# Kernel tuning notes

Hardware: AMD Instinct MI355X
Metric: run time of the kernel (lower is better)

Reference implementation:

```python
import jax, jax.numpy as jnp
import numpy as np

B, N, M, D, H = 4, 512, 4096, 256, 8
HD = D // H


def setup_inputs() -> dict:
    key = jax.random.key(0)
    ks = jax.random.split(key, 10)
    s = 1.0 / np.sqrt(D)
    return {
        "amr_feats": jax.random.normal(ks[0], (B, N, D), jnp.float32),
        "amr_pad_mask": jax.random.randint(ks[1], (B, N), 0, 2) == 1,
        "visual_feats": jax.random.normal(ks[2], (B, M, D), jnp.float32),
        "W_amr_qk": jax.random.normal(ks[3], (D, D), jnp.float32) * s,
        "W_amr_v": jax.random.normal(ks[4], (D, D), jnp.float32) * s,
        "W_vis_qk": jax.random.normal(ks[5], (D, D), jnp.float32) * s,
        "W_vis_v": jax.random.normal(ks[6], (D, D), jnp.float32) * s,
        "W_amr_out": jax.random.normal(ks[7], (D, D), jnp.float32) * s,
        "b_amr_out": jnp.zeros((D,), jnp.float32),
        "W_vis_out": jax.random.normal(ks[8], (D, D), jnp.float32) * s,
        "b_vis_out": jnp.zeros((D,), jnp.float32),
    }


def _split_heads(x):  # [b, s, d] -> [b, h, s, hd]
    b, s, _ = x.shape
    return x.reshape(b, s, H, HD).transpose(0, 2, 1, 3)


def _merge_heads(x):  # [b, h, s, hd] -> [b, s, d]
    b, _, s, _ = x.shape
    return x.transpose(0, 2, 1, 3).reshape(b, s, H * HD)


def reference(amr_feats, amr_pad_mask, visual_feats,
              W_amr_qk, W_amr_v, W_vis_qk, W_vis_v,
              W_amr_out, b_amr_out, W_vis_out, b_vis_out):
    scale = HD ** -0.5
    amr_qk = _split_heads(amr_feats @ W_amr_qk)      # [b,h,n,hd]
    vis_qk = _split_heads(visual_feats @ W_vis_qk)   # [b,h,m,hd]
    amr_v = _split_heads(amr_feats @ W_amr_v)        # [b,h,n,hd]
    vis_v = _split_heads(visual_feats @ W_vis_v)     # [b,h,m,hd]

    # shared score matrix, computed once and reused for both directions
    common = jnp.einsum('bhnc,bhmc->bhnm', amr_qk, vis_qk) * scale  # [b,h,n,m]

    # amr -> visual (visual_pads is None in the top-level forward: no mask)
    amr_vis_w = jax.nn.softmax(common, axis=-1)
    amr_feats_2 = _merge_heads(jnp.einsum('bhnm,bhmc->bhnc', amr_vis_w, vis_v))
    amr_feats_2 = amr_feats_2 @ W_amr_out + b_amr_out

    # visual -> amr, masked by amr_pad_mask
    neg = jnp.finfo(common.dtype).min
    vis_txt = jnp.where(amr_pad_mask[:, None, None, :], neg,
                        common.transpose(0, 1, 3, 2))  # [b,h,m,n]
    vis_txt_w = jax.nn.softmax(vis_txt, axis=-1)
    visual_feats_2 = _merge_heads(jnp.einsum('bhmn,bhnc->bhmc', vis_txt_w, amr_v))
    visual_feats_2 = visual_feats_2 @ W_vis_out + b_vis_out

    # text_trans == 'dot', visual_trans == 'dot'
    return amr_feats_2 * amr_feats, visual_feats * visual_feats_2
```

## Files before the change

kernel.cpp:

```cpp
#include <hip/hip_runtime.h>

#define BB 4
#define NN 512
#define MM 4096
#define DD 256
#define HH 8
#define HDD 32

typedef __attribute__((ext_vector_type(8))) short bf16x8;
typedef __attribute__((ext_vector_type(4))) float f32x4;
typedef __attribute__((ext_vector_type(4))) unsigned int u32x4;

__device__ __forceinline__ unsigned short f2b(float f) {
    union { float f; unsigned u; } v; v.f = f;
    unsigned r = v.u + 0x7fffu + ((v.u >> 16) & 1u);
    return (unsigned short)(r >> 16);
}
__device__ __forceinline__ float b2f(unsigned short u) {
    union { unsigned u; float f; } v; v.u = ((unsigned)u) << 16;
    return v.f;
}
__device__ __forceinline__ unsigned cvt_pk_bf16(float lo, float hi) {
    unsigned r;
    asm("v_cvt_pk_bf16_f32 %0, %1, %2" : "=v"(r) : "v"(lo), "v"(hi));
    return r;
}

struct WPack { const float* s[6]; unsigned short* d[6]; };
__global__ __launch_bounds__(256) void convert_w(WPack p)
{
    __shared__ unsigned short T[64][72];
    const int mat = blockIdx.x >> 4;
    const int tile = blockIdx.x & 15;
    const int kt = (tile >> 2) * 64, ct = (tile & 3) * 64;
    const int t = threadIdx.x;
    const int kl = t >> 2, cseg = (t & 3) * 16;

    const float* src = &p.s[mat][(size_t)(kt + kl) * DD + ct + cseg];
    #pragma unroll
    for (int j4 = 0; j4 < 4; ++j4) {
        const float4 f = *(const float4*)(src + j4 * 4);
        T[cseg + j4 * 4 + 0][kl] = f2b(f.x);
        T[cseg + j4 * 4 + 1][kl] = f2b(f.y);
        T[cseg + j4 * 4 + 2][kl] = f2b(f.z);
        T[cseg + j4 * 4 + 3][kl] = f2b(f.w);
    }
    __syncthreads();
    unsigned short* dst = &p.d[mat][(size_t)(ct + kl) * DD + kt + cseg];
    *(bf16x8*)dst       = *(const bf16x8*)&T[kl][cseg];
    *(bf16x8*)(dst + 8) = *(const bf16x8*)&T[kl][cseg + 8];
}

template<int OUTMODE>
__device__ __forceinline__ void gemm_tile_in(
    const float* __restrict__ A,
    const unsigned short* __restrict__ Wt,
    float outscale,
    unsigned short* __restrict__ Cb,
    unsigned short* __restrict__ VT, int SEQ,
    int r0, int c0,
    unsigned short (*As)[72], unsigned short (*Ws)[72])
{
    const int tid = threadIdx.x;
    const int lane = tid & 63, w = tid >> 6;
    const int rq = (w >> 1) * 32, cq = (w & 1) * 32;
    const int srow = tid >> 2, skc = (tid & 3) * 16;
    const int g = lane >> 4, cl = lane & 15;

    f32x4 acc[2][2] = {};

    for (int ks = 0; ks < DD; ks += 64) {
        __syncthreads();
        {
            const float* ga = &A[(size_t)(r0 + srow) * DD + ks + skc];
            const float4 f0 = *(const float4*)(ga);
            const float4 f1 = *(const float4*)(ga + 4);
            const float4 f2 = *(const float4*)(ga + 8);
            const float4 f3 = *(const float4*)(ga + 12);
            uint4 u0, u1;
            u0.x = cvt_pk_bf16(f0.x, f0.y); u0.y = cvt_pk_bf16(f0.z, f0.w);
            u0.z = cvt_pk_bf16(f1.x, f1.y); u0.w = cvt_pk_bf16(f1.z, f1.w);
            u1.x = cvt_pk_bf16(f2.x, f2.y); u1.y = cvt_pk_bf16(f2.z, f2.w);
            u1.z = cvt_pk_bf16(f3.x, f3.y); u1.w = cvt_pk_bf16(f3.z, f3.w);
            *(uint4*)&As[srow][skc]     = u0;
            *(uint4*)&As[srow][skc + 8] = u1;
            const unsigned short* gw = &Wt[(size_t)(c0 + srow) * DD + ks + skc];
            *(bf16x8*)&Ws[srow][skc]     = *(const bf16x8*)gw;
            *(bf16x8*)&Ws[srow][skc + 8] = *(const bf16x8*)(gw + 8);
        }
        __syncthreads();
        #pragma unroll
        for (int kh = 0; kh < 2; ++kh) {
            const int kk = kh * 32 + g * 8;
            const bf16x8 a0 = *(const bf16x8*)&As[rq + cl][kk];
            const bf16x8 a1 = *(const bf16x8*)&As[rq + 16 + cl][kk];
            const bf16x8 b0 = *(const bf16x8*)&Ws[cq + cl][kk];
            const bf16x8 b1 = *(const bf16x8*)&Ws[cq + 16 + cl][kk];
            acc[0][0] = __builtin_amdgcn_mfma_f32_16x16x32_bf16(a0, b0, acc[0][0], 0, 0, 0);
            acc[0][1] = __builtin_amdgcn_mfma_f32_16x16x32_bf16(a0, b1, acc[0][1], 0, 0, 0);
            acc[1][0] = __builtin_amdgcn_mfma_f32_16x16x32_bf16(a1, b0, acc[1][0], 0, 0, 0);
            acc[1][1] = __builtin_amdgcn_mfma_f32_16x16x32_bf16(a1, b1, acc[1][1], 0, 0, 0);
        }
    }

    if (OUTMODE == 0) {
        const int b0 = r0 / SEQ, mbase = r0 % SEQ;
        #pragma unroll
        for (int sr = 0; sr < 2; ++sr)
        #pragma unroll
        for (int sc = 0; sc < 2; ++sc) {
            const int col = c0 + cq + sc * 16 + cl;
            const int head = col >> 5, c32 = col & 31;
            #pragma unroll
            for (int reg = 0; reg < 4; ++reg) {
                const int m = mbase + rq + sr * 16 + g * 4 + reg;
                Cb[(((size_t)b0 * HH + head) * SEQ + m) * 32 + c32]
                    = f2b(acc[sr][sc][reg] * outscale);
            }
        }
    } else {
        __syncthreads();
        #pragma unroll
        for (int sr = 0; sr < 2; ++sr)
        #pragma unroll
        for (int sc = 0; sc < 2; ++sc) {
            const int col_local = cq + sc * 16 + cl;
            uint2 u;
            u.x = cvt_pk_bf16(acc[sr][sc][0], acc[sr][sc][1]);
            u.y = cvt_pk_bf16(acc[sr][sc][2], acc[sr][sc][3]);
            *(uint2*)&As[col_local][rq + g * 8 + sr * 4] = u;
        }
        __syncthreads();
        const int col = tid >> 2, seg = tid & 3;
        const int b = r0 / SEQ, m0 = r0 % SEQ;
        unsigned short* dst = &VT[((size_t)b * DD + c0 + col) * SEQ + m0 + seg * 16];
        *(bf16x8*)dst       = *(const bf16x8*)&As[col][seg * 16];
        *(bf16x8*)(dst + 8) = *(const bf16x8*)&As[col][seg * 16 + 8];
    }
}

struct InPack {
    const float* amr; const float* vis;
    const unsigned short *Wqa, *Wva, *Wqv, *Wvv;
    unsigned short *amr_qk, *vis_qk, *VTa, *VTv;
    float sqs;
};
__global__ __launch_bounds__(256) void gemm_in(InPack p)
{
    __shared__ unsigned short As[64][72];
    __shared__ unsigned short Ws[64][72];
    const int bx = blockIdx.x;
    const int c0 = blockIdx.y * 64;
    if (bx < 32)
        gemm_tile_in<0>(p.amr, p.Wqa, p.sqs, p.amr_qk, nullptr, NN, bx * 64, c0, As, Ws);
    else if (bx < 64)
        gemm_tile_in<2>(p.amr, p.Wva, 1.f, nullptr, p.VTa, NN, (bx - 32) * 64, c0, As, Ws);
    else if (bx < 320)
        gemm_tile_in<0>(p.vis, p.Wqv, p.sqs, p.vis_qk, nullptr, MM, (bx - 64) * 64, c0, As, Ws);
    else
        gemm_tile_in<2>(p.vis, p.Wvv, 1.f, nullptr, p.VTv, MM, (bx - 320) * 64, c0, As, Ws);
}

__device__ __forceinline__ void gemm_tile_out(
    const unsigned short* __restrict__ A,
    const unsigned short* __restrict__ Wt,
    const float* __restrict__ bias,
    const float* __restrict__ feats,
    float* __restrict__ Cf,
    int r0, int c0,
    unsigned short (*As)[72], unsigned short (*Ws)[72])
{
    const int tid = threadIdx.x;
    const int lane = tid & 63, w = tid >> 6;
    const int rq = (w >> 1) * 32, cq = (w & 1) * 32;
    const int srow = tid >> 2, skc = (tid & 3) * 16;
    const int g = lane >> 4, cl = lane & 15;

    f32x4 acc[2][2] = {};

    for (int ks = 0; ks < DD; ks += 64) {
        __syncthreads();
        {
            const unsigned short* ga = &A[(size_t)(r0 + srow) * DD + ks + skc];
            *(bf16x8*)&As[srow][skc]     = *(const bf16x8*)ga;
            *(bf16x8*)&As[srow][skc + 8] = *(const bf16x8*)(ga + 8);
            const unsigned short* gw = &Wt[(size_t)(c0 + srow) * DD + ks + skc];
            *(bf16x8*)&Ws[srow][skc]     = *(const bf16x8*)gw;
            *(bf16x8*)&Ws[srow][skc + 8] = *(const bf16x8*)(gw + 8);
        }
        __syncthreads();
        #pragma unroll
        for (int kh = 0; kh < 2; ++kh) {
            const int kk = kh * 32 + g * 8;
            const bf16x8 a0 = *(const bf16x8*)&As[rq + cl][kk];
            const bf16x8 a1 = *(const bf16x8*)&As[rq + 16 + cl][kk];
            const bf16x8 b0 = *(const bf16x8*)&Ws[cq + cl][kk];
            const bf16x8 b1 = *(const bf16x8*)&Ws[cq + 16 + cl][kk];
            acc[0][0] = __builtin_amdgcn_mfma_f32_16x16x32_bf16(a0, b0, acc[0][0], 0, 0, 0);
            acc[0][1] = __builtin_amdgcn_mfma_f32_16x16x32_bf16(a0, b1, acc[0][1], 0, 0, 0);
            acc[1][0] = __builtin_amdgcn_mfma_f32_16x16x32_bf16(a1, b0, acc[1][0], 0, 0, 0);
            acc[1][1] = __builtin_amdgcn_mfma_f32_16x16x32_bf16(a1, b1, acc[1][1], 0, 0, 0);
        }
    }

    #pragma unroll
    for (int sr = 0; sr < 2; ++sr)
    #pragma unroll
    for (int sc = 0; sc < 2; ++sc) {
        const int col = c0 + cq + sc * 16 + cl;
        #pragma unroll
        for (int reg = 0; reg < 4; ++reg) {
            const int row = r0 + rq + sr * 16 + g * 4 + reg;
            const size_t idx = (size_t)row * DD + col;
            Cf[idx] = (acc[sr][sc][reg] + bias[col]) * feats[idx];
        }
    }
}

struct OutPack {
    const unsigned short* A[2];
    const unsigned short* Wt[2];
    const float* bias[2];
    const float* feats[2];
    float* O[2];
};
__global__ __launch_bounds__(256) void gemm_out(OutPack p)
{
    __shared__ unsigned short As[64][72];
    __shared__ unsigned short Ws[64][72];
    const int bx = blockIdx.x;
    const int which = (bx < 32) ? 0 : 1;
    const int rb = (bx < 32) ? bx : bx - 32;
    gemm_tile_out(p.A[which], p.Wt[which], p.bias[which], p.feats[which],
                  p.O[which], rb * 64, blockIdx.y * 64, As, Ws);
}

template<int SEQK, int SPLIT, bool HAS_MASK>
__device__ __forceinline__ void attn_body(
    int bid,
    const unsigned short* __restrict__ Qb,
    const unsigned short* __restrict__ Kb,
    const unsigned short* __restrict__ VTb,
    const int* __restrict__ mask,
    unsigned short* __restrict__ ctx,
    float* __restrict__ Pl, unsigned short* __restrict__ PaccB,
    int NQ, float* maskadd)
{
    constexpr int KCHUNK = SEQK / SPLIT;
    constexpr int NT = KCHUNK / 64;

    const int tid = threadIdx.x;
    const int lane = tid & 63, w = tid >> 6;
    const int g = lane >> 4, cl = lane & 15;

    const int nqt = NQ / 256;
    int bi = bid;
    const int sp = bi % SPLIT; bi /= SPLIT;
    const int qt = bi % nqt;   bi /= nqt;
    const int h  = bi % HH;
    const int b  = bi / HH;
    const int q0 = qt * 256 + w * 64;
    const int kv0 = sp * KCHUNK;

    if (HAS_MASK) {
        for (int i = tid; i < SEQK; i += 256)
            maskadd[i] = mask[b * SEQK + i] ? -1e30f : 0.f;
        __syncthreads();
    }

    bf16x8 aq[4];
    #pragma unroll
    for (int qg = 0; qg < 4; ++qg)
        aq[qg] = *(const bf16x8*)
            &Qb[(((size_t)b * HH + h) * NQ + q0 + qg * 16 + cl) * 32 + g * 8];

    const unsigned short* Kp0 = Kb + (((size_t)b * HH + h) * SEQK + kv0 + cl) * 32 + g * 8;
    const unsigned short* Vp0 = VTb + ((size_t)b * DD + h * HDD + cl) * SEQK + kv0 + g * 8;

    float lsum[4] = {0.f, 0.f, 0.f, 0.f};
    f32x4 acc[4][2] = {};

    bf16x8 Kc[4], Kn[4];
    #pragma unroll
    for (int kf = 0; kf < 4; ++kf)
        Kc[kf] = *(const bf16x8*)(Kp0 + (size_t)(kf * 16) * 32);

    for (int t = 0; t < NT; ++t) {
        const int m0 = kv0 + t * 64;

        if (t + 1 < NT) {
            const unsigned short* kp = Kp0 + (size_t)((t + 1) * 64) * 32;
            #pragma unroll
            for (int kf = 0; kf < 4; ++kf)
                Kn[kf] = *(const bf16x8*)(kp + (size_t)(kf * 16) * 32);
        }

        bf16x8 vv[2][2];
        #pragma unroll
        for (int mh = 0; mh < 2; ++mh)
            #pragma unroll
            for (int sub = 0; sub < 2; ++sub)
                vv[mh][sub] = *(const bf16x8*)
                    (Vp0 + (size_t)(sub * 16) * SEQK + t * 64 + mh * 32);

        uint2 X[4][4];
        #pragma unroll
        for (int kh = 0; kh < 2; ++kh) {
            f32x4 s[4][2];
            #pragma unroll
            for (int k2 = 0; k2 < 2; ++k2) {
                const f32x4 z = {0.f, 0.f, 0.f, 0.f};
                const bf16x8 kfrag = Kc[kh * 2 + k2];
                #pragma unroll
                for (int qg = 0; qg < 4; ++qg)
                    s[qg][k2] = __builtin_amdgcn_mfma_f32_16x16x32_bf16(
                        kfrag, aq[qg], z, 0, 0, 0);
            }
            #pragma unroll
            for (int k2 = 0; k2 < 2; ++k2) {
                const int kf = kh * 2 + k2;
                f32x4 madd;
                if (HAS_MASK)
                    madd = *(const f32x4*)&maskadd[m0 + kf * 16 + g * 4];
                #pragma unroll
                for (int qg = 0; qg < 4; ++qg) {
                    const float p0 = exp2f(s[qg][k2][0] + (HAS_MASK ? madd[0] : 0.f));
                    const float p1 = exp2f(s[qg][k2][1] + (HAS_MASK ? madd[1] : 0.f));
                    const float p2 = exp2f(s[qg][k2][2] + (HAS_MASK ? madd[2] : 0.f));
                    const float p3 = exp2f(s[qg][k2][3] + (HAS_MASK ? madd[3] : 0.f));
                    lsum[qg] += (p0 + p1) + (p2 + p3);
                    X[qg][kf].x = cvt_pk_bf16(p0, p1);
                    X[qg][kf].y = cvt_pk_bf16(p2, p3);
                }
            }
        }

        #pragma unroll
        for (int mh = 0; mh < 2; ++mh) {
            union { u32x4 u; bf16x8 b; } pa[4];
            #pragma unroll
            for (int qg = 0; qg < 4; ++qg) {
                pa[qg].u[0] = X[qg][mh * 2].x;
                pa[qg].u[1] = X[qg][mh * 2].y;
                pa[qg].u[2] = X[qg][mh * 2 + 1].x;
                pa[qg].u[3] = X[qg][mh * 2 + 1].y;
            }
            #pragma unroll
            for (int sub = 0; sub < 2; ++sub)
                #pragma unroll
                for (int qg = 0; qg < 4; ++qg)
                    acc[qg][sub] = __builtin_amdgcn_mfma_f32_16x16x32_bf16(
                        pa[qg].b, vv[mh][sub], acc[qg][sub], 0, 0, 0);
        }

        #pragma unroll
        for (int kf = 0; kf < 4; ++kf) Kc[kf] = Kn[kf];
    }

    #pragma unroll
    for (int qg = 0; qg < 4; ++qg) {
        lsum[qg] += __shfl_xor(lsum[qg], 16);
        lsum[qg] += __shfl_xor(lsum[qg], 32);
    }

    if (SPLIT > 1) {
        const int pb = bid;
        #pragma unroll
        for (int qg = 0; qg < 4; ++qg) {
            #pragma unroll
            for (int sub = 0; sub < 2; ++sub)
                #pragma unroll
                for (int reg = 0; reg < 4; ++reg) {
                    const int wq = w * 64 + qg * 16 + g * 4 + reg;
                    PaccB[((size_t)pb * 256 + wq) * 32 + sub * 16 + cl]
                        = f2b(acc[qg][sub][reg]);
                }
            if (g == 0)
                Pl[(size_t)pb * 256 + w * 64 + qg * 16 + cl] = lsum[qg];
        }
    } else {
        float linv[4][4];
        #pragma unroll
        for (int qg = 0; qg < 4; ++qg)
            #pragma unroll
            for (int reg = 0; reg < 4; ++reg)
                linv[qg][reg] = __shfl(lsum[qg], g * 4 + reg);
        #pragma unroll
        for (int qg = 0; qg < 4; ++qg)
            #pragma unroll
            for (int sub = 0; sub < 2; ++sub)
                #pragma unroll
                for (int reg = 0; reg < 4; ++reg) {
                    const int q = q0 + qg * 16 + g * 4 + reg;
                    ctx[((size_t)b * NQ + q) * DD + h * HDD + sub * 16 + cl]
                        = f2b(acc[qg][sub][reg] / linv[qg][reg]);
                }
    }
}

__global__ __launch_bounds__(256) void attn_fused(
    const unsigned short* __restrict__ amr_qk,
    const unsigned short* __restrict__ vis_qk,
    const unsigned short* __restrict__ VT_vis,
    const unsigned short* __restrict__ VT_amr,
    const int* __restrict__ mask,
    unsigned short* __restrict__ ctx1,
    float* __restrict__ Pl, unsigned short* __restrict__ PaccB)
{
    __shared__ float maskadd[NN];
    if ((blockIdx.x & 1) == 0) {
        attn_body<MM, 8, false>(blockIdx.x >> 1, amr_qk, vis_qk, VT_vis, nullptr,
                                nullptr, Pl, PaccB, NN, maskadd);
    } else {
        attn_body<NN, 1, true>(blockIdx.x >> 1, vis_qk, amr_qk, VT_amr, mask,
                               ctx1, nullptr, nullptr, MM, maskadd);
    }
}

__global__ __launch_bounds__(256) void combine_split(
    const float* __restrict__ Pl, const unsigned short* __restrict__ PaccB,
    unsigned short* __restrict__ ctx)
{
    const int q = threadIdx.x;
    const int bqt = blockIdx.x;
    const int qt = bqt & 1, h = (bqt >> 1) & 7, b = bqt >> 4;
    const int pb0 = bqt * 8;

    float denom = 0.f;
    float o[32] = {};
    #pragma unroll
    for (int sp = 0; sp < 8; ++sp) {
        const size_t base = ((size_t)(pb0 + sp) * 256 + q) * 32;
        #pragma unroll
        for (int c8 = 0; c8 < 4; ++c8) {
            const bf16x8 a = *(const bf16x8*)&PaccB[base + c8 * 8];
            #pragma unroll
            for (int j = 0; j < 8; ++j)
                o[c8 * 8 + j] += b2f((unsigned short)a[j]);
        }
        denom += Pl[(size_t)(pb0 + sp) * 256 + q];
    }
    const float inv = 1.f / denom;

    unsigned short* dst = &ctx[((size_t)b * NN + qt * 256 + q) * DD + h * HDD];
    #pragma unroll
    for (int j4 = 0; j4 < 8; ++j4) {
        ushort4 u;
        u.x = f2b(o[j4 * 4 + 0] * inv); u.y = f2b(o[j4 * 4 + 1] * inv);
        u.z = f2b(o[j4 * 4 + 2] * inv); u.w = f2b(o[j4 * 4 + 3] * inv);
        *(ushort4*)(dst + j4 * 4) = u;
    }
}

extern "C" void kernel_launch(void* const* d_in, const int* in_sizes, int n_in,
                              void* d_out, int out_size, void* d_ws, size_t ws_size,
                              hipStream_t stream)
{
    const float* amr_feats    = (const float*)d_in[0];
    const int*   amr_pad_mask = (const int*)d_in[1];
    const float* visual_feats = (const float*)d_in[2];
    const float* W_amr_qk     = (const float*)d_in[3];
    const float* W_amr_v      = (const float*)d_in[4];
    const float* W_vis_qk     = (const float*)d_in[5];
    const float* W_vis_v      = (const float*)d_in[6];
    const float* W_amr_out    = (const float*)d_in[7];
    const float* b_amr_out    = (const float*)d_in[8];
    const float* W_vis_out    = (const float*)d_in[9];
    const float* b_vis_out    = (const float*)d_in[10];

    unsigned short* ws = (unsigned short*)d_ws;
    unsigned short* Wt_amr_qk  = ws;
    unsigned short* Wt_amr_v   = ws + 65536;
    unsigned short* Wt_vis_qk  = ws + 131072;
    unsigned short* Wt_vis_v   = ws + 196608;
    unsigned short* Wt_amr_out = ws + 262144;
    unsigned short* Wt_vis_out = ws + 327680;
    unsigned short* amr_qk_b   = ws + 393216;
    unsigned short* VT_amr     = ws + 917504;
    unsigned short* vis_qk_b   = ws + 1441792;
    unsigned short* VT_vis     = ws + 5636096;
    unsigned short* ctx0_b     = ws + 9830400;
    unsigned short* ctx1_b     = ws + 10354688;
    float* Pl                  = (float*)(ws + 14548992);
    unsigned short* PaccB      = ws + 15073280;

    float* out0 = (float*)d_out;
    float* out1 = out0 + (size_t)BB * NN * DD;

    const float SQS = 0.50500976f;

    WPack wp;
    wp.s[0] = W_amr_qk;  wp.d[0] = Wt_amr_qk;
    wp.s[1] = W_amr_v;   wp.d[1] = Wt_amr_v;
    wp.s[2] = W_vis_qk;  wp.d[2] = Wt_vis_qk;
    wp.s[3] = W_vis_v;   wp.d[3] = Wt_vis_v;
    wp.s[4] = W_amr_out; wp.d[4] = Wt_amr_out;
    wp.s[5] = W_vis_out; wp.d[5] = Wt_vis_out;
    convert_w<<<96, 256, 0, stream>>>(wp);

    InPack ip;
    ip.amr = amr_feats; ip.vis = visual_feats;
    ip.Wqa = Wt_amr_qk; ip.Wva = Wt_amr_v;
    ip.Wqv = Wt_vis_qk; ip.Wvv = Wt_vis_v;
    ip.amr_qk = amr_qk_b; ip.vis_qk = vis_qk_b;
    ip.VTa = VT_amr; ip.VTv = VT_vis;
    ip.sqs = SQS;
    gemm_in<<<dim3(576, 4), 256, 0, stream>>>(ip);

    attn_fused<<<1024, 256, 0, stream>>>(
        amr_qk_b, vis_qk_b, VT_vis, VT_amr, amr_pad_mask, ctx1_b, Pl, PaccB);
    combine_split<<<64, 256, 0, stream>>>(Pl, PaccB, ctx0_b);

    OutPack op;
    op.A[0] = ctx0_b; op.Wt[0] = Wt_amr_out; op.bias[0] = b_amr_out;
    op.feats[0] = amr_feats;    op.O[0] = out0;
    op.A[1] = ctx1_b; op.Wt[1] = Wt_vis_out; op.bias[1] = b_vis_out;
    op.feats[1] = visual_feats; op.O[1] = out1;
    gemm_out<<<dim3(288, 4), 256, 0, stream>>>(op);
}
```

Before: 94.35 us.

## Compute softmax row sums via MFMA with keep vector and pre-mask V rows

Replaces the scalar per-lane accumulation of exp values and the cross-lane shuffle reduction with an extra MFMA per tile that multiplies P by a bf16 ones (or keep-mask) fragment, so the denominator comes out of the matrix unit. Masking of padded keys moves out of the attention loop: V rows for padded tokens are zeroed in the input GEMM, and a permuted bf16 keep vector built by an extra grid column supplies the masked denominator. This removes the shared-memory mask table, its sync and the per-element mask adds, at the cost of extra MFMAs, a global load per tile, and denominators summed from bf16-rounded probabilities.

```diff
diff --git a/kernel.cpp b/kernel.cpp
--- a/kernel.cpp
+++ b/kernel.cpp
@@ -58,6 +58,7 @@
     float outscale,
     unsigned short* __restrict__ Cb,
     unsigned short* __restrict__ VT, int SEQ,
+    const int* __restrict__ rowmask,
     int r0, int c0,
     unsigned short (*As)[72], unsigned short (*Ws)[72])
 {
@@ -119,6 +120,18 @@
             }
         }
     } else {
+        const int b0 = r0 / SEQ, mbase = r0 % SEQ;
+        if (rowmask != nullptr) {
+            #pragma unroll
+            for (int sr = 0; sr < 2; ++sr)
+                #pragma unroll
+                for (int reg = 0; reg < 4; ++reg) {
+                    const int m = mbase + rq + sr * 16 + g * 4 + reg;
+                    const float k = rowmask[b0 * SEQ + m] ? 0.f : 1.f;
+                    acc[sr][0][reg] *= k;
+                    acc[sr][1][reg] *= k;
+                }
+        }
         __syncthreads();
         #pragma unroll
         for (int sr = 0; sr < 2; ++sr)
@@ -132,8 +145,7 @@
         }
         __syncthreads();
         const int col = tid >> 2, seg = tid & 3;
-        const int b = r0 / SEQ, m0 = r0 % SEQ;
-        unsigned short* dst = &VT[((size_t)b * DD + c0 + col) * SEQ + m0 + seg * 16];
+        unsigned short* dst = &VT[((size_t)b0 * DD + c0 + col) * SEQ + mbase + seg * 16];
         *(bf16x8*)dst       = *(const bf16x8*)&As[col][seg * 16];
         *(bf16x8*)(dst + 8) = *(const bf16x8*)&As[col][seg * 16 + 8];
     }
@@ -143,6 +155,8 @@
     const float* amr; const float* vis;
     const unsigned short *Wqa, *Wva, *Wqv, *Wvv;
     unsigned short *amr_qk, *vis_qk, *VTa, *VTv;
+    const int* mask;
+    unsigned short* keepP;
     float sqs;
 };
 __global__ __launch_bounds__(256) void gemm_in(InPack p)
@@ -152,13 +166,24 @@
     const int bx = blockIdx.x;
     const int c0 = blockIdx.y * 64;
     if (bx < 32)
-        gemm_tile_in<0>(p.amr, p.Wqa, p.sqs, p.amr_qk, nullptr, NN, bx * 64, c0, As, Ws);
+        gemm_tile_in<0>(p.amr, p.Wqa, p.sqs, p.amr_qk, nullptr, NN, nullptr, bx * 64, c0, As, Ws);
     else if (bx < 64)
-        gemm_tile_in<2>(p.amr, p.Wva, 1.f, nullptr, p.VTa, NN, (bx - 32) * 64, c0, As, Ws);
+        gemm_tile_in<2>(p.amr, p.Wva, 1.f, nullptr, p.VTa, NN, p.mask, (bx - 32) * 64, c0, As, Ws);
     else if (bx < 320)
-        gemm_tile_in<0>(p.vis, p.Wqv, p.sqs, p.vis_qk, nullptr, MM, (bx - 64) * 64, c0, As, Ws);
-    else
-        gemm_tile_in<2>(p.vis, p.Wvv, 1.f, nullptr, p.VTv, MM, (bx - 320) * 64, c0, As, Ws);
+        gemm_tile_in<0>(p.vis, p.Wqv, p.sqs, p.vis_qk, nullptr, MM, nullptr, (bx - 64) * 64, c0, As, Ws);
+    else if (bx < 576)
+        gemm_tile_in<2>(p.vis, p.Wvv, 1.f, nullptr, p.VTv, MM, nullptr, (bx - 320) * 64, c0, As, Ws);
+    else if (blockIdx.y == 0) {
+        #pragma unroll
+        for (int k8 = 0; k8 < 8; ++k8) {
+            const int idx = k8 * 256 + threadIdx.x;
+            const int m = idx & (NN - 1);
+            const int r = m & 31;
+            const int pp = ((r & 15) >> 2) * 8 + (r >> 4) * 4 + (r & 3);
+            p.keepP[(idx & ~(NN - 1)) | (m & ~31) | pp]
+                = p.mask[idx] ? (unsigned short)0 : (unsigned short)0x3F80;
+        }
+    }
 }
 
 __device__ __forceinline__ void gemm_tile_out(
@@ -235,16 +260,16 @@
                   p.O[which], rb * 64, blockIdx.y * 64, As, Ws);
 }
 
-template<int SEQK, int SPLIT, bool HAS_MASK>
+template<int SEQK, int SPLIT, bool HAS_KEEP>
 __device__ __forceinline__ void attn_body(
     int bid,
     const unsigned short* __restrict__ Qb,
     const unsigned short* __restrict__ Kb,
     const unsigned short* __restrict__ VTb,
-    const int* __restrict__ mask,
+    const unsigned short* __restrict__ keepP,
     unsigned short* __restrict__ ctx,
     float* __restrict__ Pl, unsigned short* __restrict__ PaccB,
-    int NQ, float* maskadd)
+    int NQ)
 {
     constexpr int KCHUNK = SEQK / SPLIT;
     constexpr int NT = KCHUNK / 64;
@@ -262,12 +287,6 @@
     const int q0 = qt * 256 + w * 64;
     const int kv0 = sp * KCHUNK;
 
-    if (HAS_MASK) {
-        for (int i = tid; i < SEQK; i += 256)
-            maskadd[i] = mask[b * SEQK + i] ? -1e30f : 0.f;
-        __syncthreads();
-    }
-
     bf16x8 aq[4];
     #pragma unroll
     for (int qg = 0; qg < 4; ++qg)
@@ -276,9 +295,14 @@
 
     const unsigned short* Kp0 = Kb + (((size_t)b * HH + h) * SEQK + kv0 + cl) * 32 + g * 8;
     const unsigned short* Vp0 = VTb + ((size_t)b * DD + h * HDD + cl) * SEQK + kv0 + g * 8;
-
-    float lsum[4] = {0.f, 0.f, 0.f, 0.f};
+    const unsigned short* Op0 = HAS_KEEP ? (keepP + (size_t)b * SEQK + kv0 + g * 8) : nullptr;
+
+    union { u32x4 u; bf16x8 b; } onesc;
+    onesc.u[0] = 0x3F803F80u; onesc.u[1] = 0x3F803F80u;
+    onesc.u[2] = 0x3F803F80u; onesc.u[3] = 0x3F803F80u;
+
     f32x4 acc[4][2] = {};
+    f32x4 acc_l[4] = {};
 
     bf16x8 Kc[4], Kn[4];
     #pragma unroll
@@ -286,8 +310,6 @@
         Kc[kf] = *(const bf16x8*)(Kp0 + (size_t)(kf * 16) * 32);
 
     for (int t = 0; t < NT; ++t) {
-        const int m0 = kv0 + t * 64;
-
         if (t + 1 < NT) {
             const unsigned short* kp = Kp0 + (size_t)((t + 1) * 64) * 32;
             #pragma unroll
@@ -302,6 +324,15 @@
             for (int sub = 0; sub < 2; ++sub)
                 vv[mh][sub] = *(const bf16x8*)
                     (Vp0 + (size_t)(sub * 16) * SEQK + t * 64 + mh * 32);
+
+        bf16x8 ofrag[2];
+        if (HAS_KEEP) {
+            ofrag[0] = *(const bf16x8*)(Op0 + t * 64);
+            ofrag[1] = *(const bf16x8*)(Op0 + t * 64 + 32);
+        } else {
+            ofrag[0] = onesc.b;
+            ofrag[1] = onesc.b;
+        }
 
         uint2 X[4][4];
         #pragma unroll
@@ -319,16 +350,12 @@
             #pragma unroll
             for (int k2 = 0; k2 < 2; ++k2) {
                 const int kf = kh * 2 + k2;
-                f32x4 madd;
-                if (HAS_MASK)
-                    madd = *(const f32x4*)&maskadd[m0 + kf * 16 + g * 4];
                 #pragma unroll
                 for (int qg = 0; qg < 4; ++qg) {
-                    const float p0 = exp2f(s[qg][k2][0] + (HAS_MASK ? madd[0] : 0.f));
-                    const float p1 = exp2f(s[qg][k2][1] + (HAS_MASK ? madd[1] : 0.f));
-                    const float p2 = exp2f(s[qg][k2][2] + (HAS_MASK ? madd[2] : 0.f));
-                    const float p3 = exp2f(s[qg][k2][3] + (HAS_MASK ? madd[3] : 0.f));
-                    lsum[qg] += (p0 + p1) + (p2 + p3);
+                    const float p0 = exp2f(s[qg][k2][0]);
+                    const float p1 = exp2f(s[qg][k2][1]);
+                    const float p2 = exp2f(s[qg][k2][2]);
+                    const float p3 = exp2f(s[qg][k2][3]);
                     X[qg][kf].x = cvt_pk_bf16(p0, p1);
                     X[qg][kf].y = cvt_pk_bf16(p2, p3);
                 }
@@ -351,16 +378,14 @@
                 for (int qg = 0; qg < 4; ++qg)
                     acc[qg][sub] = __builtin_amdgcn_mfma_f32_16x16x32_bf16(
                         pa[qg].b, vv[mh][sub], acc[qg][sub], 0, 0, 0);
+            #pragma unroll
+            for (int qg = 0; qg < 4; ++qg)
+                acc_l[qg] = __builtin_amdgcn_mfma_f32_16x16x32_bf16(
+                    pa[qg].b, ofrag[mh], acc_l[qg], 0, 0, 0);
         }
 
         #pragma unroll
         for (int kf = 0; kf < 4; ++kf) Kc[kf] = Kn[kf];
-    }
-
-    #pragma unroll
-    for (int qg = 0; qg < 4; ++qg) {
-        lsum[qg] += __shfl_xor(lsum[qg], 16);
-        lsum[qg] += __shfl_xor(lsum[qg], 32);
     }
 
     if (SPLIT > 1) {
@@ -375,16 +400,14 @@
                     PaccB[((size_t)pb * 256 + wq) * 32 + sub * 16 + cl]
                         = f2b(acc[qg][sub][reg]);
                 }
-            if (g == 0)
-                Pl[(size_t)pb * 256 + w * 64 + qg * 16 + cl] = lsum[qg];
+            if (cl == 0) {
+                #pragma unroll
+                for (int reg = 0; reg < 4; ++reg)
+                    Pl[(size_t)pb * 256 + w * 64 + qg * 16 + g * 4 + reg]
+                        = acc_l[qg][reg];
+            }
         }
     } else {
-        float linv[4][4];
-        #pragma unroll
-        for (int qg = 0; qg < 4; ++qg)
-            #pragma unroll
-            for (int reg = 0; reg < 4; ++reg)
-                linv[qg][reg] = __shfl(lsum[qg], g * 4 + reg);
         #pragma unroll
         for (int qg = 0; qg < 4; ++qg)
             #pragma unroll
@@ -393,7 +416,7 @@
                 for (int reg = 0; reg < 4; ++reg) {
                     const int q = q0 + qg * 16 + g * 4 + reg;
                     ctx[((size_t)b * NQ + q) * DD + h * HDD + sub * 16 + cl]
-                        = f2b(acc[qg][sub][reg] / linv[qg][reg]);
+                        = f2b(acc[qg][sub][reg] / acc_l[qg][reg]);
                 }
     }
 }
@@ -403,17 +426,16 @@
     const unsigned short* __restrict__ vis_qk,
     const unsigned short* __restrict__ VT_vis,
     const unsigned short* __restrict__ VT_amr,
-    const int* __restrict__ mask,
+    const unsigned short* __restrict__ keepP,
     unsigned short* __restrict__ ctx1,
     float* __restrict__ Pl, unsigned short* __restrict__ PaccB)
 {
-    __shared__ float maskadd[NN];
     if ((blockIdx.x & 1) == 0) {
         attn_body<MM, 8, false>(blockIdx.x >> 1, amr_qk, vis_qk, VT_vis, nullptr,
-                                nullptr, Pl, PaccB, NN, maskadd);
+                                nullptr, Pl, PaccB, NN);
     } else {
-        attn_body<NN, 1, true>(blockIdx.x >> 1, vis_qk, amr_qk, VT_amr, mask,
-                               ctx1, nullptr, nullptr, MM, maskadd);
+        attn_body<NN, 1, true>(blockIdx.x >> 1, vis_qk, amr_qk, VT_amr, keepP,
+                               ctx1, nullptr, nullptr, MM);
     }
 }
 
@@ -483,6 +505,7 @@
     unsigned short* ctx1_b     = ws + 10354688;
     float* Pl                  = (float*)(ws + 14548992);
     unsigned short* PaccB      = ws + 15073280;
+    unsigned short* keepP      = ws + 19267584;
 
     float* out0 = (float*)d_out;
     float* out1 = out0 + (size_t)BB * NN * DD;
@@ -504,11 +527,12 @@
     ip.Wqv = Wt_vis_qk; ip.Wvv = Wt_vis_v;
     ip.amr_qk = amr_qk_b; ip.vis_qk = vis_qk_b;
     ip.VTa = VT_amr; ip.VTv = VT_vis;
+    ip.mask = amr_pad_mask; ip.keepP = keepP;
     ip.sqs = SQS;
-    gemm_in<<<dim3(576, 4), 256, 0, stream>>>(ip);
+    gemm_in<<<dim3(577, 4), 256, 0, stream>>>(ip);
 
     attn_fused<<<1024, 256, 0, stream>>>(
-        amr_qk_b, vis_qk_b, VT_vis, VT_amr, amr_pad_mask, ctx1_b, Pl, PaccB);
+        amr_qk_b, vis_qk_b, VT_vis, VT_amr, keepP, ctx1_b, Pl, PaccB);
     combine_split<<<64, 256, 0, stream>>>(Pl, PaccB, ctx0_b);
 
     OutPack op;
```

Result: faster. 91.85 us (-2.6%).
